# Performance work log

Hardware: AMD Instinct MI355X
Metric: run time of the kernel (lower is better)

The kernel has to match this reference:

```python
import jax, jax.numpy as jnp
import numpy as np

D = 128          # node_state_dim
N_NODES = 5000
WINDOW = 10
N_TOTAL = WINDOW * N_NODES
E = 131072       # structural (int) edges
T = 2            # message passing steps
HID = 1024


def setup_inputs() -> dict:
    key = jax.random.key(0)
    ks = jax.random.split(key, 20)
    ie = jax.random.randint(ks[0], (E, 3), 0, N_NODES, dtype=jnp.int32)
    int_edges = jnp.stack([ie[:, 0] % WINDOW, ie[:, 1], ie[:, 2]], axis=1)
    nodes = jax.random.randint(ks[1], (N_NODES,), 0, 10, dtype=jnp.int32)

    def init(k, shape, scale=0.05):
        return (jax.random.normal(k, shape, jnp.float32) * scale)

    params = dict(
        embed_table=init(ks[2], (10, D)),
        msg_W1=init(ks[3], (2 * D, HID)), msg_b1=jnp.zeros((HID,), jnp.float32),
        msg_W2=init(ks[4], (HID, D)), msg_b2=jnp.zeros((D,), jnp.float32),
        gru_int_W=init(ks[5], (D, 3 * D)), gru_int_U=init(ks[6], (D, 3 * D)),
        gru_int_b=jnp.zeros((2, 3 * D), jnp.float32),
        gru_temp_W=init(ks[7], (D, 3 * D)), gru_temp_U=init(ks[8], (D, 3 * D)),
        gru_temp_b=jnp.zeros((2, 3 * D), jnp.float32),
        ro_W1=init(ks[9], (D, HID)), ro_b1=jnp.zeros((HID,), jnp.float32),
        ro_W2=init(ks[10], (HID, 512)), ro_b2=jnp.zeros((512,), jnp.float32),
        ro_W3=init(ks[11], (512, 10)), ro_b3=jnp.zeros((10,), jnp.float32),
    )
    return {"int_edges": int_edges, "nodes": nodes, **params}


def _temp_edges():
    fwd_src = np.arange(0, N_TOTAL - N_NODES)
    fwd_dst = fwd_src + N_NODES
    bwd_src = np.arange(N_NODES, N_TOTAL)
    bwd_dst = bwd_src - N_NODES
    src = jnp.asarray(np.concatenate([fwd_src, bwd_src]), jnp.int32)
    dst = jnp.asarray(np.concatenate([fwd_dst, bwd_dst]), jnp.int32)
    return src, dst


def _gru(x, h, W, U, b):
    # Keras GRUCell, reset_after=True. x,h: [N,D]; W,U: [D,3D]; b: [2,3D]
    xg = x @ W + b[0]
    hg = h @ U + b[1]
    xz, xr, xh = jnp.split(xg, 3, axis=-1)
    hz, hr, hh = jnp.split(hg, 3, axis=-1)
    z = jax.nn.sigmoid(xz + hz)
    r = jax.nn.sigmoid(xr + hr)
    hcand = jnp.tanh(xh + r * hh)
    return z * h + (1.0 - z) * hcand


def _msg(x, W1, b1, W2, b2):
    # Dense(1024,relu) -> Dropout(inference: identity) -> Dense(D,relu)
    return jax.nn.relu(jax.nn.relu(x @ W1 + b1) @ W2 + b2)


def _seg_mean(x, idx, n):
    s = jax.ops.segment_sum(x, idx, num_segments=n)
    c = jax.ops.segment_sum(jnp.ones((x.shape[0],), x.dtype), idx, num_segments=n)
    return jnp.where(c[:, None] > 0, s / jnp.maximum(c, 1.0)[:, None], 0.0)


def reference(int_edges, nodes, embed_table, msg_W1, msg_b1, msg_W2, msg_b2,
              gru_int_W, gru_int_U, gru_int_b, gru_temp_W, gru_temp_U, gru_temp_b,
              ro_W1, ro_b1, ro_W2, ro_b2, ro_W3, ro_b3):
    node_idx = int_edges[:, 0] * N_NODES + int_edges[:, 1]        # [E]
    neigh_idx = int_edges[:, 0] * N_NODES + int_edges[:, 2]       # [E]
    t_src, t_dst = _temp_edges()

    h = embed_table[nodes]                                        # [n_nodes, D]
    h = jnp.repeat(h, WINDOW, axis=0)                             # [N_TOTAL, D]

    for _ in range(T):
        # structural edges
        m_in = jnp.concatenate([h[node_idx], h[neigh_idx]], axis=1)   # [E, 2D]
        m = _msg(m_in, msg_W1, msg_b1, msg_W2, msg_b2)                # [E, D]
        agg = _seg_mean(m, neigh_idx, N_TOTAL)                        # [N_TOTAL, D]
        h = _gru(agg, h, gru_int_W, gru_int_U, gru_int_b)
        # temporal edges
        tm_in = jnp.concatenate([h[t_src], h[t_dst]], axis=1)
        tm = _msg(tm_in, msg_W1, msg_b1, msg_W2, msg_b2)
        tagg = _seg_mean(tm, t_dst, N_TOTAL)
        h = _gru(tagg, h, gru_temp_W, gru_temp_U, gru_temp_b)

    # readout on first frame's nodes
    x = h[:N_NODES]
    x = jax.nn.relu(x @ ro_W1 + ro_b1)
    x = jax.nn.relu(x @ ro_W2 + ro_b2)
    return jax.nn.softmax(x @ ro_W3 + ro_b3, axis=-1)
```

## Files before the change

### kernel.cpp

```cpp
#include <hip/hip_runtime.h>
#include <math.h>

#define D 128
#define N_NODES 5000
#define WINDOW 10
#define N_TOTAL 50000
#define NE_INT 131072
#define NE_TMP 90000
#define NE_FWD (N_TOTAL - N_NODES)
#define HID 1024

typedef short bf16x8 __attribute__((ext_vector_type(8)));
typedef float f32x4 __attribute__((ext_vector_type(4)));

#define SA 264
#define SH 136
#define SK 136
#define SCAN_B 256

static __device__ __forceinline__ short f2bf(float f) {
    union { float f; unsigned u; } v; v.f = f;
    unsigned r = v.u + 0x7fffu + ((v.u >> 16) & 1u);
    return (short)(r >> 16);
}
static __device__ __forceinline__ float bf2f(short s) {
    union { unsigned u; float f; } v;
    v.u = ((unsigned)(unsigned short)s) << 16;
    return v.f;
}

__global__ void k_tcvt(const float* __restrict__ in, short* __restrict__ out, int K, int N) {
    int i = blockIdx.x * blockDim.x + threadIdx.x;
    if (i >= N * K) return;
    int n = i / K, k = i - n * K;
    out[i] = f2bf(in[(size_t)k * N + n]);
}

__global__ void k_init_h(const int* __restrict__ nodes, const float* __restrict__ embed,
                         float* __restrict__ h32, short* __restrict__ h16) {
    int i = blockIdx.x * blockDim.x + threadIdx.x;
    if (i >= N_TOTAL * D) return;
    int row = i >> 7;
    int c = i & 127;
    int n = nodes[row / WINDOW];
    float v = embed[n * D + c];
    h32[i] = v;
    h16[i] = f2bf(v);
}

__global__ void k_build_int_edges(const int* __restrict__ ie, int* __restrict__ src,
                                  int* __restrict__ dst, int* __restrict__ icnt) {
    int e = blockIdx.x * blockDim.x + threadIdx.x;
    if (e >= NE_INT) return;
    int t = ie[e * 3 + 0], a = ie[e * 3 + 1], b = ie[e * 3 + 2];
    int d = t * N_NODES + b;
    src[e] = t * N_NODES + a;
    dst[e] = d;
    atomicAdd(&icnt[d], 1);
}

__global__ void k_build_tmp_edges(int* __restrict__ src, int* __restrict__ dst) {
    int e = blockIdx.x * blockDim.x + threadIdx.x;
    if (e >= NE_TMP) return;
    int s, d;
    if (e < NE_FWD) { s = e; d = e + N_NODES; }
    else { int q = e - NE_FWD; s = q + N_NODES; d = q; }
    src[e] = s;
    dst[e] = d;
}

__global__ void k_scan_partial(const int* __restrict__ cnt, int* __restrict__ rowstart,
                               int* __restrict__ btot, int n) {
    __shared__ int s[SCAN_B];
    int tid = threadIdx.x;
    int i = blockIdx.x * SCAN_B + tid;
    int v = (i < n) ? cnt[i] : 0;
    s[tid] = v;
    __syncthreads();
    for (int off = 1; off < SCAN_B; off <<= 1) {
        int x = (tid >= off) ? s[tid - off] : 0;
        __syncthreads();
        s[tid] += x;
        __syncthreads();
    }
    if (i < n) rowstart[i] = s[tid] - v;
    if (tid == SCAN_B - 1) btot[blockIdx.x] = s[tid];
}

__global__ void k_scan_block(int* __restrict__ btot, int nb) {
    __shared__ int s[SCAN_B];
    int tid = threadIdx.x;
    int v = (tid < nb) ? btot[tid] : 0;
    s[tid] = v;
    __syncthreads();
    for (int off = 1; off < SCAN_B; off <<= 1) {
        int x = (tid >= off) ? s[tid - off] : 0;
        __syncthreads();
        s[tid] += x;
        __syncthreads();
    }
    if (tid < nb) btot[tid] = s[tid] - v;
}

__global__ void k_scan_add(int* __restrict__ rowstart, const int* __restrict__ btot,
                           int* __restrict__ cursor, int n, int total) {
    int i = blockIdx.x * blockDim.x + threadIdx.x;
    if (i < n) {
        int v = rowstart[i] + btot[i >> 8];
        rowstart[i] = v;
        cursor[i] = v;
    }
    if (i == 0) rowstart[n] = total;
}

__global__ void k_fill_csr(const int* __restrict__ dst, int nE, int* __restrict__ cursor,
                           int* __restrict__ eidx) {
    int e = blockIdx.x * blockDim.x + threadIdx.x;
    if (e >= nE) return;
    int p = atomicAdd(&cursor[dst[e]], 1);
    eidx[p] = e;
}

__global__ void __launch_bounds__(256, 2) k_msg_mfma(
    const short* __restrict__ h16, const int* __restrict__ src, const int* __restrict__ dst,
    int nE, const short* __restrict__ W1T, const float* __restrict__ b1,
    const short* __restrict__ W2T, const float* __restrict__ b2,
    short* __restrict__ m)
{
    __shared__ short Ain[64 * SA];
    __shared__ short Hid[64 * SH];

    int t = threadIdx.x;
    int e0 = blockIdx.x * 64;

    {
        int r = t >> 2, q = t & 3;
        int e = e0 + r;
        int ec = (e < nE) ? e : (nE - 1);
        int s = src[ec], d = dst[ec];
        const uint4* ps = (const uint4*)(h16 + (size_t)s * D);
        const uint4* pd = (const uint4*)(h16 + (size_t)d * D);
        uint4* ao = (uint4*)(Ain + r * SA);
#pragma unroll
        for (int i = 0; i < 8; ++i) {
            int g = i * 4 + q;
            ao[g] = (i < 4) ? ps[g] : pd[g - 16];
        }
    }
    __syncthreads();

    int w = t >> 6, lane = t & 63;
    int lm = lane & 15, lk = lane >> 4;

    f32x4 c2[2][4];
#pragma unroll
    for (int cs = 0; cs < 2; ++cs) {
        int out0 = w * 32 + cs * 16 + lk * 4;
#pragma unroll
        for (int et = 0; et < 4; ++et)
#pragma unroll
            for (int rg = 0; rg < 4; ++rg) c2[cs][et][rg] = b2[out0 + rg];
    }

    for (int hc = 0; hc < 8; ++hc) {
        f32x4 c1[2][4];
#pragma unroll
        for (int cs = 0; cs < 2; ++cs) {
            int ch0 = hc * 128 + (2 * w + cs) * 16 + lk * 4;
#pragma unroll
            for (int et = 0; et < 4; ++et)
#pragma unroll
                for (int rg = 0; rg < 4; ++rg) c1[cs][et][rg] = b1[ch0 + rg];
        }
#pragma unroll
        for (int kk = 0; kk < 8; ++kk) {
            int ko = kk * 32 + lk * 8;
            bf16x8 a0 = *(const bf16x8*)(W1T + (size_t)(hc * 128 + (2 * w) * 16 + lm) * 256 + ko);
            bf16x8 a1 = *(const bf16x8*)(W1T + (size_t)(hc * 128 + (2 * w + 1) * 16 + lm) * 256 + ko);
            bf16x8 bf[4];
#pragma unroll
            for (int et = 0; et < 4; ++et)
                bf[et] = *(const bf16x8*)(Ain + (et * 16 + lm) * SA + ko);
#pragma unroll
            for (int et = 0; et < 4; ++et) {
                c1[0][et] = __builtin_amdgcn_mfma_f32_16x16x32_bf16(a0, bf[et], c1[0][et], 0, 0, 0);
                c1[1][et] = __builtin_amdgcn_mfma_f32_16x16x32_bf16(a1, bf[et], c1[1][et], 0, 0, 0);
            }
        }
        __syncthreads();
#pragma unroll
        for (int cs = 0; cs < 2; ++cs) {
            int ch_in = (2 * w + cs) * 16 + lk * 4;
#pragma unroll
            for (int et = 0; et < 4; ++et) {
                int edge = et * 16 + lm;
                short4 sv;
                sv.x = f2bf(fmaxf(c1[cs][et][0], 0.f));
                sv.y = f2bf(fmaxf(c1[cs][et][1], 0.f));
                sv.z = f2bf(fmaxf(c1[cs][et][2], 0.f));
                sv.w = f2bf(fmaxf(c1[cs][et][3], 0.f));
                *(short4*)(Hid + edge * SH + ch_in) = sv;
            }
        }
        __syncthreads();
#pragma unroll
        for (int kk = 0; kk < 4; ++kk) {
            int ko = kk * 32 + lk * 8;
            bf16x8 a0 = *(const bf16x8*)(W2T + (size_t)(w * 32 + lm) * 1024 + hc * 128 + ko);
            bf16x8 a1 = *(const bf16x8*)(W2T + (size_t)(w * 32 + 16 + lm) * 1024 + hc * 128 + ko);
            bf16x8 bf[4];
#pragma unroll
            for (int et = 0; et < 4; ++et)
                bf[et] = *(const bf16x8*)(Hid + (et * 16 + lm) * SH + ko);
#pragma unroll
            for (int et = 0; et < 4; ++et) {
                c2[0][et] = __builtin_amdgcn_mfma_f32_16x16x32_bf16(a0, bf[et], c2[0][et], 0, 0, 0);
                c2[1][et] = __builtin_amdgcn_mfma_f32_16x16x32_bf16(a1, bf[et], c2[1][et], 0, 0, 0);
            }
        }
    }

#pragma unroll
    for (int et = 0; et < 4; ++et) {
        int edge = et * 16 + lm;
        int e = e0 + edge;
        if (e >= nE) continue;
        short* rowp = m + (size_t)e * 128;
#pragma unroll
        for (int cs = 0; cs < 2; ++cs) {
            int out0 = w * 32 + cs * 16 + lk * 4;
            short4 sv;
            sv.x = f2bf(fmaxf(c2[cs][et][0], 0.f));
            sv.y = f2bf(fmaxf(c2[cs][et][1], 0.f));
            sv.z = f2bf(fmaxf(c2[cs][et][2], 0.f));
            sv.w = f2bf(fmaxf(c2[cs][et][3], 0.f));
            *(short4*)(rowp + out0) = sv;
        }
    }
}

__global__ void __launch_bounds__(256, 2) k_gru_mfma(
    const short* __restrict__ m, const int* __restrict__ rowstart,
    const int* __restrict__ eidx, int mode,
    float* __restrict__ h32, short* __restrict__ h16,
    const short* __restrict__ WT, const short* __restrict__ UT,
    const float* __restrict__ b)
{
    __shared__ short Ax[64 * SK];
    __shared__ short Hx[64 * SK];
    int t = threadIdx.x;
    int r0 = blockIdx.x * 64;

    {
        int r = t >> 2, q = t & 3;
        int row = r0 + r;
        int rc = (row < N_TOTAL) ? row : (N_TOTAL - 1);
        const uint4* hp = (const uint4*)(h16 + (size_t)rc * D);
        uint4* hxo = (uint4*)(Hx + r * SK);
#pragma unroll
        for (int i = 0; i < 4; ++i) hxo[q * 4 + i] = hp[q * 4 + i];

        float acc[32];
#pragma unroll
        for (int i = 0; i < 32; ++i) acc[i] = 0.f;
        int deg = 0;
        if (row < N_TOTAL) {
            if (mode == 0) {
                int s0 = rowstart[row], s1 = rowstart[row + 1];
                deg = s1 - s0;
                for (int p = s0; p < s1; ++p) {
                    int e = eidx[p];
                    const uint4* mp = (const uint4*)(m + (size_t)e * 128 + q * 32);
#pragma unroll
                    for (int i = 0; i < 4; ++i) {
                        uint4 v = mp[i];
                        const short* sp = (const short*)&v;
#pragma unroll
                        for (int j = 0; j < 8; ++j) acc[i * 8 + j] += bf2f(sp[j]);
                    }
                }
            } else {
                if (row >= N_NODES) {
                    const uint4* mp = (const uint4*)(m + (size_t)(row - N_NODES) * 128 + q * 32);
                    ++deg;
#pragma unroll
                    for (int i = 0; i < 4; ++i) {
                        uint4 v = mp[i];
                        const short* sp = (const short*)&v;
#pragma unroll
                        for (int j = 0; j < 8; ++j) acc[i * 8 + j] += bf2f(sp[j]);
                    }
                }
                if (row < NE_FWD) {
                    const uint4* mp = (const uint4*)(m + (size_t)(NE_FWD + row) * 128 + q * 32);
                    ++deg;
#pragma unroll
                    for (int i = 0; i < 4; ++i) {
                        uint4 v = mp[i];
                        const short* sp = (const short*)&v;
#pragma unroll
                        for (int j = 0; j < 8; ++j) acc[i * 8 + j] += bf2f(sp[j]);
                    }
                }
            }
        }
        float inv = (deg > 0) ? 1.f / (float)deg : 0.f;
        uint4* axp = (uint4*)(Ax + r * SK + q * 32);
#pragma unroll
        for (int i = 0; i < 4; ++i) {
            union { uint4 u; short s[8]; } pk;
#pragma unroll
            for (int j = 0; j < 8; ++j) pk.s[j] = f2bf(acc[i * 8 + j] * inv);
            axp[i] = pk.u;
        }
    }
    __syncthreads();

    int w = t >> 6, lane = t & 63;
    int lm = lane & 15, lk = lane >> 4;

    for (int g = 0; g < 8; ++g) {
        int ch = g * 16 + lm;
        f32x4 cxz, cxr, cxh, chz, chr_, chh;
#pragma unroll
        for (int rg = 0; rg < 4; ++rg) {
            cxz[rg] = b[ch];        chz[rg] = b[384 + ch];
            cxr[rg] = b[128 + ch];  chr_[rg] = b[384 + 128 + ch];
            cxh[rg] = b[256 + ch];  chh[rg] = b[384 + 256 + ch];
        }
#pragma unroll
        for (int kk = 0; kk < 4; ++kk) {
            int ko = kk * 32 + lk * 8;
            bf16x8 ax = *(const bf16x8*)(Ax + (w * 16 + lm) * SK + ko);
            bf16x8 hx = *(const bf16x8*)(Hx + (w * 16 + lm) * SK + ko);
            bf16x8 bz = *(const bf16x8*)(WT + (size_t)(ch) * 128 + ko);
            bf16x8 br = *(const bf16x8*)(WT + (size_t)(128 + ch) * 128 + ko);
            bf16x8 bh = *(const bf16x8*)(WT + (size_t)(256 + ch) * 128 + ko);
            bf16x8 uz = *(const bf16x8*)(UT + (size_t)(ch) * 128 + ko);
            bf16x8 ur = *(const bf16x8*)(UT + (size_t)(128 + ch) * 128 + ko);
            bf16x8 uh = *(const bf16x8*)(UT + (size_t)(256 + ch) * 128 + ko);
            cxz = __builtin_amdgcn_mfma_f32_16x16x32_bf16(ax, bz, cxz, 0, 0, 0);
            cxr = __builtin_amdgcn_mfma_f32_16x16x32_bf16(ax, br, cxr, 0, 0, 0);
            cxh = __builtin_amdgcn_mfma_f32_16x16x32_bf16(ax, bh, cxh, 0, 0, 0);
            chz = __builtin_amdgcn_mfma_f32_16x16x32_bf16(hx, uz, chz, 0, 0, 0);
            chr_ = __builtin_amdgcn_mfma_f32_16x16x32_bf16(hx, ur, chr_, 0, 0, 0);
            chh = __builtin_amdgcn_mfma_f32_16x16x32_bf16(hx, uh, chh, 0, 0, 0);
        }
#pragma unroll
        for (int rg = 0; rg < 4; ++rg) {
            int row = r0 + w * 16 + lk * 4 + rg;
            if (row >= N_TOTAL) continue;
            float z = 1.f / (1.f + expf(-(cxz[rg] + chz[rg])));
            float r_ = 1.f / (1.f + expf(-(cxr[rg] + chr_[rg])));
            float hcv = tanhf(cxh[rg] + r_ * chh[rg]);
            size_t idx = (size_t)row * D + ch;
            float hold = h32[idx];
            float hnew = z * hold + (1.f - z) * hcv;
            h32[idx] = hnew;
            h16[idx] = f2bf(hnew);
        }
    }
}

__global__ void __launch_bounds__(256, 2) k_ro_mfma(
    const short* __restrict__ A16, const short* __restrict__ BT,
    const float* __restrict__ bias, float* __restrict__ C32, short* __restrict__ C16,
    int M, int N, int K)
{
    __shared__ short As[64 * SK];
    int t = threadIdx.x;
    int mb = blockIdx.y * 64;
    int nb = blockIdx.x * 128;
    int w = t >> 6, lane = t & 63;
    int lm = lane & 15, lk = lane >> 4;

    f32x4 acc[8];
#pragma unroll
    for (int nt = 0; nt < 8; ++nt) {
        float bv = bias[nb + nt * 16 + lm];
        acc[nt][0] = bv; acc[nt][1] = bv; acc[nt][2] = bv; acc[nt][3] = bv;
    }

    for (int kc = 0; kc < K; kc += 128) {
        __syncthreads();
        {
            int r = t >> 2, q = t & 3;
            int row = mb + r;
            int rc = (row < M) ? row : (M - 1);
            const uint4* ap = (const uint4*)(A16 + (size_t)rc * K + kc);
            uint4* ao = (uint4*)(As + r * SK);
#pragma unroll
            for (int i = 0; i < 4; ++i) ao[i * 4 + q] = ap[i * 4 + q];
        }
        __syncthreads();
#pragma unroll
        for (int kk = 0; kk < 4; ++kk) {
            int ko = kk * 32 + lk * 8;
            bf16x8 a = *(const bf16x8*)(As + (w * 16 + lm) * SK + ko);
#pragma unroll
            for (int nt = 0; nt < 8; ++nt) {
                bf16x8 bfr = *(const bf16x8*)(BT + (size_t)(nb + nt * 16 + lm) * K + kc + ko);
                acc[nt] = __builtin_amdgcn_mfma_f32_16x16x32_bf16(a, bfr, acc[nt], 0, 0, 0);
            }
        }
    }
#pragma unroll
    for (int nt = 0; nt < 8; ++nt) {
        int col = nb + nt * 16 + lm;
#pragma unroll
        for (int rg = 0; rg < 4; ++rg) {
            int row = mb + w * 16 + lk * 4 + rg;
            if (row >= M) continue;
            float v = fmaxf(acc[nt][rg], 0.f);
            if (C32) C32[(size_t)row * N + col] = v;
            if (C16) C16[(size_t)row * N + col] = f2bf(v);
        }
    }
}

__global__ void __launch_bounds__(64) k_logits_softmax(
    const float* __restrict__ r2, const float* __restrict__ W3,
    const float* __restrict__ b3, float* __restrict__ out)
{
    int row = blockIdx.x;
    int t = threadIdx.x;
    float p[10];
#pragma unroll
    for (int j = 0; j < 10; ++j) p[j] = 0.f;
    for (int k = t; k < 512; k += 64) {
        float v = r2[(size_t)row * 512 + k];
#pragma unroll
        for (int j = 0; j < 10; ++j) p[j] += v * W3[k * 10 + j];
    }
#pragma unroll
    for (int j = 0; j < 10; ++j) {
        float s = p[j];
        for (int off = 32; off > 0; off >>= 1) s += __shfl_down(s, off);
        p[j] = s;
    }
    if (t == 0) {
        float mx = -1e30f;
#pragma unroll
        for (int j = 0; j < 10; ++j) { p[j] += b3[j]; mx = fmaxf(mx, p[j]); }
        float sum = 0.f;
#pragma unroll
        for (int j = 0; j < 10; ++j) { p[j] = expf(p[j] - mx); sum += p[j]; }
        float inv = 1.f / sum;
#pragma unroll
        for (int j = 0; j < 10; ++j) out[(size_t)row * 10 + j] = p[j] * inv;
    }
}

extern "C" void kernel_launch(void* const* d_in, const int* in_sizes, int n_in,
                              void* d_out, int out_size, void* d_ws, size_t ws_size,
                              hipStream_t stream)
{
    const int*   ie    = (const int*)d_in[0];
    const int*   nodes = (const int*)d_in[1];
    const float* embed = (const float*)d_in[2];
    const float* mW1   = (const float*)d_in[3];
    const float* mb1   = (const float*)d_in[4];
    const float* mW2   = (const float*)d_in[5];
    const float* mb2   = (const float*)d_in[6];
    const float* giW   = (const float*)d_in[7];
    const float* giU   = (const float*)d_in[8];
    const float* gib   = (const float*)d_in[9];
    const float* gtW   = (const float*)d_in[10];
    const float* gtU   = (const float*)d_in[11];
    const float* gtb   = (const float*)d_in[12];
    const float* rW1   = (const float*)d_in[13];
    const float* rb1   = (const float*)d_in[14];
    const float* rW2   = (const float*)d_in[15];
    const float* rb2   = (const float*)d_in[16];
    const float* rW3   = (const float*)d_in[17];
    const float* rb3   = (const float*)d_in[18];
    float* out = (float*)d_out;

    char* ws = (char*)d_ws;
    size_t off = 0;
    auto alloc = [&](size_t bytes) {
        void* p = ws + off;
        off += (bytes + 255) & ~(size_t)255;
        return p;
    };
    float* h32   = (float*)alloc((size_t)N_TOTAL * D * 4);
    short* h16   = (short*)alloc((size_t)N_TOTAL * D * 2);
    short* m     = (short*)alloc((size_t)NE_INT * 128 * 2);
    int*   icnt  = (int*)alloc((size_t)N_TOTAL * 4);
    int*   rowst = (int*)alloc((size_t)(N_TOTAL + 1) * 4);
    int*   btot  = (int*)alloc(256 * 4);
    int*   curs  = (int*)alloc((size_t)N_TOTAL * 4);
    int*   eidx  = (int*)alloc((size_t)NE_INT * 4);
    int*   srcA  = (int*)alloc((size_t)NE_INT * 4);
    int*   dstA  = (int*)alloc((size_t)NE_INT * 4);
    int*   srcT  = (int*)alloc((size_t)NE_TMP * 4);
    int*   dstT  = (int*)alloc((size_t)NE_TMP * 4);
    short* mW1T  = (short*)alloc((size_t)HID * 256 * 2);
    short* mW2T  = (short*)alloc((size_t)D * HID * 2);
    short* giWT  = (short*)alloc((size_t)384 * D * 2);
    short* giUT  = (short*)alloc((size_t)384 * D * 2);
    short* gtWT  = (short*)alloc((size_t)384 * D * 2);
    short* gtUT  = (short*)alloc((size_t)384 * D * 2);
    short* rW1T  = (short*)alloc((size_t)HID * D * 2);
    short* rW2T  = (short*)alloc((size_t)512 * HID * 2);
    short* r1_16 = (short*)alloc((size_t)N_NODES * HID * 2);
    float* r2_32 = (float*)alloc((size_t)N_NODES * 512 * 4);

    auto tc = [&](const float* in, short* o, int K, int N) {
        k_tcvt<<<(N * K + 255) / 256, 256, 0, stream>>>(in, o, K, N);
    };
    tc(mW1, mW1T, 256, HID);
    tc(mW2, mW2T, HID, D);
    tc(giW, giWT, D, 384);
    tc(giU, giUT, D, 384);
    tc(gtW, gtWT, D, 384);
    tc(gtU, gtUT, D, 384);
    tc(rW1, rW1T, D, HID);
    tc(rW2, rW2T, HID, 512);

    hipMemsetAsync(icnt, 0, (size_t)N_TOTAL * 4, stream);
    k_init_h<<<(N_TOTAL * D + 255) / 256, 256, 0, stream>>>(nodes, embed, h32, h16);
    k_build_int_edges<<<(NE_INT + 255) / 256, 256, 0, stream>>>(ie, srcA, dstA, icnt);
    k_build_tmp_edges<<<(NE_TMP + 255) / 256, 256, 0, stream>>>(srcT, dstT);
    int nb = (N_TOTAL + SCAN_B - 1) / SCAN_B;
    k_scan_partial<<<nb, SCAN_B, 0, stream>>>(icnt, rowst, btot, N_TOTAL);
    k_scan_block<<<1, SCAN_B, 0, stream>>>(btot, nb);
    k_scan_add<<<nb, SCAN_B, 0, stream>>>(rowst, btot, curs, N_TOTAL, NE_INT);
    k_fill_csr<<<(NE_INT + 255) / 256, 256, 0, stream>>>(dstA, NE_INT, curs, eidx);

    int gmsgA = (NE_INT + 63) / 64;
    int gmsgT = (NE_TMP + 63) / 64;
    int ggru = (N_TOTAL + 63) / 64;
    for (int it = 0; it < 2; ++it) {
        k_msg_mfma<<<gmsgA, 256, 0, stream>>>(h16, srcA, dstA, NE_INT, mW1T, mb1, mW2T, mb2, m);
        k_gru_mfma<<<ggru, 256, 0, stream>>>(m, rowst, eidx, 0, h32, h16, giWT, giUT, gib);

        k_msg_mfma<<<gmsgT, 256, 0, stream>>>(h16, srcT, dstT, NE_TMP, mW1T, mb1, mW2T, mb2, m);
        k_gru_mfma<<<ggru, 256, 0, stream>>>(m, rowst, eidx, 1, h32, h16, gtWT, gtUT, gtb);
    }

    dim3 g1(HID / 128, (N_NODES + 63) / 64);
    k_ro_mfma<<<g1, 256, 0, stream>>>(h16, rW1T, rb1, (float*)nullptr, r1_16, N_NODES, HID, D);
    dim3 g2(512 / 128, (N_NODES + 63) / 64);
    k_ro_mfma<<<g2, 256, 0, stream>>>(r1_16, rW2T, rb2, r2_32, (short*)nullptr, N_NODES, 512, HID);
    k_logits_softmax<<<N_NODES, 64, 0, stream>>>(r2_32, rW3, rb3, out);
}
```

Baseline: 1.299 ms.

## Precompute per-node first-layer projections and gather them per edge

Splits the first message-MLP layer as [h_src,h_dst]@W1 = h_src@W1a + h_dst@W1b. Both halves are computed once per node into a 50000x2048 bf16 buffer, so each edge only gathers two 1024-wide rows, adds them and applies ReLU before the second GEMM. Structural edges are processed in CSR (dst-sorted) order, so the GRU aggregation reads messages contiguously without the eidx indirection. The change trades roughly 2.5x fewer first-layer FLOPs for a 200MB intermediate buffer that is written and then gathered from. It also adds an extra bf16 rounding before the sum, and falls back to the old path if the workspace is too small.

```diff
diff --git a/kernel.cpp b/kernel.cpp
--- a/kernel.cpp
+++ b/kernel.cpp
@@ -121,6 +121,178 @@
     eidx[p] = e;
 }
 
+__global__ void __launch_bounds__(256, 3) k_h12_mfma(
+    const short* __restrict__ h16, const short* __restrict__ W1cT,
+    const float* __restrict__ b1, short* __restrict__ H12)
+{
+    __shared__ short As[128 * SK];
+    int t = threadIdx.x;
+    int nb = blockIdx.x * 128;
+    int mb = blockIdx.y * 128;
+
+    {
+        int r = t >> 1, q = t & 1;
+        int row = mb + r;
+        int rc = (row < N_TOTAL) ? row : (N_TOTAL - 1);
+        const uint4* ap = (const uint4*)(h16 + (size_t)rc * D);
+        uint4* ao = (uint4*)(As + r * SK);
+#pragma unroll
+        for (int i = 0; i < 8; ++i) ao[q * 8 + i] = ap[q * 8 + i];
+    }
+    __syncthreads();
+
+    int w = t >> 6, lane = t & 63, lm = lane & 15, lk = lane >> 4;
+
+    f32x4 acc[2][8];
+#pragma unroll
+    for (int nt = 0; nt < 8; ++nt) {
+        int col = nb + nt * 16 + lm;
+        float bv = (col < HID) ? b1[col] : 0.f;
+#pragma unroll
+        for (int mt = 0; mt < 2; ++mt)
+#pragma unroll
+            for (int rg = 0; rg < 4; ++rg) acc[mt][nt][rg] = bv;
+    }
+#pragma unroll
+    for (int kk = 0; kk < 4; ++kk) {
+        int ko = kk * 32 + lk * 8;
+        bf16x8 a0 = *(const bf16x8*)(As + (w * 32 + lm) * SK + ko);
+        bf16x8 a1 = *(const bf16x8*)(As + (w * 32 + 16 + lm) * SK + ko);
+#pragma unroll
+        for (int nt = 0; nt < 8; ++nt) {
+            bf16x8 bfr = *(const bf16x8*)(W1cT + (size_t)(nb + nt * 16 + lm) * D + ko);
+            acc[0][nt] = __builtin_amdgcn_mfma_f32_16x16x32_bf16(a0, bfr, acc[0][nt], 0, 0, 0);
+            acc[1][nt] = __builtin_amdgcn_mfma_f32_16x16x32_bf16(a1, bfr, acc[1][nt], 0, 0, 0);
+        }
+    }
+#pragma unroll
+    for (int mt = 0; mt < 2; ++mt)
+#pragma unroll
+        for (int rg = 0; rg < 4; ++rg) {
+            int row = mb + w * 32 + mt * 16 + lk * 4 + rg;
+            if (row >= N_TOTAL) continue;
+            short* op = H12 + (size_t)row * 2048 + nb;
+#pragma unroll
+            for (int nt = 0; nt < 8; ++nt)
+                op[nt * 16 + lm] = f2bf(acc[mt][nt][rg]);
+        }
+}
+
+__global__ void __launch_bounds__(256, 3) k_msg2_mfma(
+    const short* __restrict__ H12, const int* __restrict__ perm,
+    const int* __restrict__ src, const int* __restrict__ dst, int nE,
+    const short* __restrict__ W2T, const float* __restrict__ b2,
+    short* __restrict__ m)
+{
+    __shared__ short S[2][64 * SH];
+    __shared__ int es[64], ed[64];
+    int t = threadIdx.x;
+    int p0 = blockIdx.x * 64;
+
+    if (t < 64) {
+        int p = p0 + t;
+        int pc = (p < nE) ? p : (nE - 1);
+        int e = perm ? perm[pc] : pc;
+        es[t] = src[e];
+        ed[t] = dst[e];
+    }
+    __syncthreads();
+
+    int w = t >> 6, lane = t & 63, lm = lane & 15, lk = lane >> 4;
+    int r = t >> 2, q = t & 3;
+    const short* p1 = H12 + (size_t)es[r] * 2048 + q * 32;
+    const short* p2 = H12 + (size_t)ed[r] * 2048 + 1024 + q * 32;
+
+    uint4 ra[4], rb[4];
+#pragma unroll
+    for (int i = 0; i < 4; ++i) {
+        ra[i] = *(const uint4*)(p1 + i * 8);
+        rb[i] = *(const uint4*)(p2 + i * 8);
+    }
+
+    f32x4 c2[2][4];
+#pragma unroll
+    for (int cs = 0; cs < 2; ++cs) {
+        int out0 = w * 32 + cs * 16 + lk * 4;
+#pragma unroll
+        for (int et = 0; et < 4; ++et)
+#pragma unroll
+            for (int rg = 0; rg < 4; ++rg) c2[cs][et][rg] = b2[out0 + rg];
+    }
+
+    {
+        uint4* sp = (uint4*)(S[0] + r * SH + q * 32);
+#pragma unroll
+        for (int i = 0; i < 4; ++i) {
+            union { uint4 u; short s[8]; } pa, pb, po;
+            pa.u = ra[i]; pb.u = rb[i];
+#pragma unroll
+            for (int j = 0; j < 8; ++j)
+                po.s[j] = f2bf(fmaxf(bf2f(pa.s[j]) + bf2f(pb.s[j]), 0.f));
+            sp[i] = po.u;
+        }
+    }
+
+    for (int hc = 0; hc < 8; ++hc) {
+        int cur = hc & 1;
+        __syncthreads();
+        if (hc < 7) {
+            const short* q1 = p1 + (hc + 1) * 128;
+            const short* q2 = p2 + (hc + 1) * 128;
+#pragma unroll
+            for (int i = 0; i < 4; ++i) {
+                ra[i] = *(const uint4*)(q1 + i * 8);
+                rb[i] = *(const uint4*)(q2 + i * 8);
+            }
+        }
+#pragma unroll
+        for (int kk = 0; kk < 4; ++kk) {
+            int ko = kk * 32 + lk * 8;
+            bf16x8 a0 = *(const bf16x8*)(W2T + (size_t)(w * 32 + lm) * 1024 + hc * 128 + ko);
+            bf16x8 a1 = *(const bf16x8*)(W2T + (size_t)(w * 32 + 16 + lm) * 1024 + hc * 128 + ko);
+            bf16x8 bf[4];
+#pragma unroll
+            for (int et = 0; et < 4; ++et)
+                bf[et] = *(const bf16x8*)(S[cur] + (et * 16 + lm) * SH + ko);
+#pragma unroll
+            for (int et = 0; et < 4; ++et) {
+                c2[0][et] = __builtin_amdgcn_mfma_f32_16x16x32_bf16(a0, bf[et], c2[0][et], 0, 0, 0);
+                c2[1][et] = __builtin_amdgcn_mfma_f32_16x16x32_bf16(a1, bf[et], c2[1][et], 0, 0, 0);
+            }
+        }
+        if (hc < 7) {
+            uint4* sp = (uint4*)(S[cur ^ 1] + r * SH + q * 32);
+#pragma unroll
+            for (int i = 0; i < 4; ++i) {
+                union { uint4 u; short s[8]; } pa, pb, po;
+                pa.u = ra[i]; pb.u = rb[i];
+#pragma unroll
+                for (int j = 0; j < 8; ++j)
+                    po.s[j] = f2bf(fmaxf(bf2f(pa.s[j]) + bf2f(pb.s[j]), 0.f));
+                sp[i] = po.u;
+            }
+        }
+    }
+
+#pragma unroll
+    for (int et = 0; et < 4; ++et) {
+        int edge = et * 16 + lm;
+        int p = p0 + edge;
+        if (p >= nE) continue;
+        short* rowp = m + (size_t)p * 128;
+#pragma unroll
+        for (int cs = 0; cs < 2; ++cs) {
+            int out0 = w * 32 + cs * 16 + lk * 4;
+            short4 sv;
+            sv.x = f2bf(fmaxf(c2[cs][et][0], 0.f));
+            sv.y = f2bf(fmaxf(c2[cs][et][1], 0.f));
+            sv.z = f2bf(fmaxf(c2[cs][et][2], 0.f));
+            sv.w = f2bf(fmaxf(c2[cs][et][3], 0.f));
+            *(short4*)(rowp + out0) = sv;
+        }
+    }
+}
+
 __global__ void __launch_bounds__(256, 2) k_msg_mfma(
     const short* __restrict__ h16, const int* __restrict__ src, const int* __restrict__ dst,
     int nE, const short* __restrict__ W1T, const float* __restrict__ b1,
@@ -241,7 +413,7 @@
 
 __global__ void __launch_bounds__(256, 2) k_gru_mfma(
     const short* __restrict__ m, const int* __restrict__ rowstart,
-    const int* __restrict__ eidx, int mode,
+    const int* __restrict__ midx, int mode,
     float* __restrict__ h32, short* __restrict__ h16,
     const short* __restrict__ WT, const short* __restrict__ UT,
     const float* __restrict__ b)
@@ -269,7 +441,7 @@
                 int s0 = rowstart[row], s1 = rowstart[row + 1];
                 deg = s1 - s0;
                 for (int p = s0; p < s1; ++p) {
-                    int e = eidx[p];
+                    int e = midx ? midx[p] : p;
                     const uint4* mp = (const uint4*)(m + (size_t)e * 128 + q * 32);
 #pragma unroll
                     for (int i = 0; i < 4; ++i) {
@@ -505,6 +677,11 @@
     short* rW2T  = (short*)alloc((size_t)512 * HID * 2);
     short* r1_16 = (short*)alloc((size_t)N_NODES * HID * 2);
     float* r2_32 = (float*)alloc((size_t)N_NODES * 512 * 4);
+    short* W1cT  = (short*)alloc((size_t)2048 * D * 2);
+
+    size_t h12_bytes = (size_t)N_TOTAL * 2048 * 2;
+    bool useH12 = (off + h12_bytes <= ws_size);
+    short* H12 = useH12 ? (short*)alloc(h12_bytes) : nullptr;
 
     auto tc = [&](const float* in, short* o, int K, int N) {
         k_tcvt<<<(N * K + 255) / 256, 256, 0, stream>>>(in, o, K, N);
@@ -517,6 +694,10 @@
     tc(gtU, gtUT, D, 384);
     tc(rW1, rW1T, D, HID);
     tc(rW2, rW2T, HID, 512);
+    if (useH12) {
+        tc(mW1, W1cT, D, HID);
+        tc(mW1 + (size_t)D * HID, W1cT + (size_t)HID * D, D, HID);
+    }
 
     hipMemsetAsync(icnt, 0, (size_t)N_TOTAL * 4, stream);
     k_init_h<<<(N_TOTAL * D + 255) / 256, 256, 0, stream>>>(nodes, embed, h32, h16);
@@ -531,12 +712,23 @@
     int gmsgA = (NE_INT + 63) / 64;
     int gmsgT = (NE_TMP + 63) / 64;
     int ggru = (N_TOTAL + 63) / 64;
+    dim3 gh12(2048 / 128, (N_TOTAL + 127) / 128);
     for (int it = 0; it < 2; ++it) {
-        k_msg_mfma<<<gmsgA, 256, 0, stream>>>(h16, srcA, dstA, NE_INT, mW1T, mb1, mW2T, mb2, m);
-        k_gru_mfma<<<ggru, 256, 0, stream>>>(m, rowst, eidx, 0, h32, h16, giWT, giUT, gib);
-
-        k_msg_mfma<<<gmsgT, 256, 0, stream>>>(h16, srcT, dstT, NE_TMP, mW1T, mb1, mW2T, mb2, m);
-        k_gru_mfma<<<ggru, 256, 0, stream>>>(m, rowst, eidx, 1, h32, h16, gtWT, gtUT, gtb);
+        if (useH12) {
+            k_h12_mfma<<<gh12, 256, 0, stream>>>(h16, W1cT, mb1, H12);
+            k_msg2_mfma<<<gmsgA, 256, 0, stream>>>(H12, eidx, srcA, dstA, NE_INT, mW2T, mb2, m);
+            k_gru_mfma<<<ggru, 256, 0, stream>>>(m, rowst, (const int*)nullptr, 0, h32, h16, giWT, giUT, gib);
+
+            k_h12_mfma<<<gh12, 256, 0, stream>>>(h16, W1cT, mb1, H12);
+            k_msg2_mfma<<<gmsgT, 256, 0, stream>>>(H12, (const int*)nullptr, srcT, dstT, NE_TMP, mW2T, mb2, m);
+            k_gru_mfma<<<ggru, 256, 0, stream>>>(m, rowst, (const int*)nullptr, 1, h32, h16, gtWT, gtUT, gtb);
+        } else {
+            k_msg_mfma<<<gmsgA, 256, 0, stream>>>(h16, srcA, dstA, NE_INT, mW1T, mb1, mW2T, mb2, m);
+            k_gru_mfma<<<ggru, 256, 0, stream>>>(m, rowst, eidx, 0, h32, h16, giWT, giUT, gib);
+
+            k_msg_mfma<<<gmsgT, 256, 0, stream>>>(h16, srcT, dstT, NE_TMP, mW1T, mb1, mW2T, mb2, m);
+            k_gru_mfma<<<ggru, 256, 0, stream>>>(m, rowst, eidx, 1, h32, h16, gtWT, gtUT, gtb);
+        }
     }
 
     dim3 g1(HID / 128, (N_NODES + 63) / 64);
```

Result: no change. 1.297 ms (-0.2%).

## Software-pipeline message MLP layers and scatter messages into CSR order

Applied to the files above, without the earlier changes.

The message kernel now computes the first-layer MFMA block for hidden chunk hc+1 interleaved with the second-layer MFMAs for chunk hc. This is meant to hide the dependency stall between the two GEMM stages. Message rows are also written straight into CSR slot order through a precomputed position map, so the GRU aggregation reads contiguous rows instead of going through eidx. The bf16 unpacking in aggregation now uses 32-bit shifts and masks. The costs are higher register pressure from keeping two accumulator sets live, and scattered stores in the message kernel.

```diff
diff --git a/kernel.cpp b/kernel.cpp
--- a/kernel.cpp
+++ b/kernel.cpp
@@ -27,6 +27,12 @@
     union { unsigned u; float f; } v;
     v.u = ((unsigned)(unsigned short)s) << 16;
     return v.f;
+}
+static __device__ __forceinline__ float lo_bf(unsigned u) {
+    union { unsigned u; float f; } v; v.u = u << 16; return v.f;
+}
+static __device__ __forceinline__ float hi_bf(unsigned u) {
+    union { unsigned u; float f; } v; v.u = u & 0xffff0000u; return v.f;
 }
 
 __global__ void k_tcvt(const float* __restrict__ in, short* __restrict__ out, int K, int N) {
@@ -114,16 +120,17 @@
 }
 
 __global__ void k_fill_csr(const int* __restrict__ dst, int nE, int* __restrict__ cursor,
-                           int* __restrict__ eidx) {
+                           int* __restrict__ pmap) {
     int e = blockIdx.x * blockDim.x + threadIdx.x;
     if (e >= nE) return;
     int p = atomicAdd(&cursor[dst[e]], 1);
-    eidx[p] = e;
+    pmap[e] = p;
 }
 
 __global__ void __launch_bounds__(256, 2) k_msg_mfma(
     const short* __restrict__ h16, const int* __restrict__ src, const int* __restrict__ dst,
-    int nE, const short* __restrict__ W1T, const float* __restrict__ b1,
+    const int* __restrict__ pmap, int nE,
+    const short* __restrict__ W1T, const float* __restrict__ b1,
     const short* __restrict__ W2T, const float* __restrict__ b2,
     short* __restrict__ m)
 {
@@ -162,31 +169,32 @@
             for (int rg = 0; rg < 4; ++rg) c2[cs][et][rg] = b2[out0 + rg];
     }
 
+    f32x4 c1[2][4];
+#pragma unroll
+    for (int cs = 0; cs < 2; ++cs) {
+        int ch0 = (2 * w + cs) * 16 + lk * 4;
+#pragma unroll
+        for (int et = 0; et < 4; ++et)
+#pragma unroll
+            for (int rg = 0; rg < 4; ++rg) c1[cs][et][rg] = b1[ch0 + rg];
+    }
+#pragma unroll
+    for (int kk = 0; kk < 8; ++kk) {
+        int ko = kk * 32 + lk * 8;
+        bf16x8 a0 = *(const bf16x8*)(W1T + (size_t)((2 * w) * 16 + lm) * 256 + ko);
+        bf16x8 a1 = *(const bf16x8*)(W1T + (size_t)((2 * w + 1) * 16 + lm) * 256 + ko);
+        bf16x8 bf[4];
+#pragma unroll
+        for (int et = 0; et < 4; ++et)
+            bf[et] = *(const bf16x8*)(Ain + (et * 16 + lm) * SA + ko);
+#pragma unroll
+        for (int et = 0; et < 4; ++et) {
+            c1[0][et] = __builtin_amdgcn_mfma_f32_16x16x32_bf16(a0, bf[et], c1[0][et], 0, 0, 0);
+            c1[1][et] = __builtin_amdgcn_mfma_f32_16x16x32_bf16(a1, bf[et], c1[1][et], 0, 0, 0);
+        }
+    }
+
     for (int hc = 0; hc < 8; ++hc) {
-        f32x4 c1[2][4];
-#pragma unroll
-        for (int cs = 0; cs < 2; ++cs) {
-            int ch0 = hc * 128 + (2 * w + cs) * 16 + lk * 4;
-#pragma unroll
-            for (int et = 0; et < 4; ++et)
-#pragma unroll
-                for (int rg = 0; rg < 4; ++rg) c1[cs][et][rg] = b1[ch0 + rg];
-        }
-#pragma unroll
-        for (int kk = 0; kk < 8; ++kk) {
-            int ko = kk * 32 + lk * 8;
-            bf16x8 a0 = *(const bf16x8*)(W1T + (size_t)(hc * 128 + (2 * w) * 16 + lm) * 256 + ko);
-            bf16x8 a1 = *(const bf16x8*)(W1T + (size_t)(hc * 128 + (2 * w + 1) * 16 + lm) * 256 + ko);
-            bf16x8 bf[4];
-#pragma unroll
-            for (int et = 0; et < 4; ++et)
-                bf[et] = *(const bf16x8*)(Ain + (et * 16 + lm) * SA + ko);
-#pragma unroll
-            for (int et = 0; et < 4; ++et) {
-                c1[0][et] = __builtin_amdgcn_mfma_f32_16x16x32_bf16(a0, bf[et], c1[0][et], 0, 0, 0);
-                c1[1][et] = __builtin_amdgcn_mfma_f32_16x16x32_bf16(a1, bf[et], c1[1][et], 0, 0, 0);
-            }
-        }
         __syncthreads();
 #pragma unroll
         for (int cs = 0; cs < 2; ++cs) {
@@ -203,19 +211,45 @@
             }
         }
         __syncthreads();
-#pragma unroll
-        for (int kk = 0; kk < 4; ++kk) {
+
+        if (hc < 7) {
+#pragma unroll
+            for (int cs = 0; cs < 2; ++cs) {
+                int ch0 = (hc + 1) * 128 + (2 * w + cs) * 16 + lk * 4;
+#pragma unroll
+                for (int et = 0; et < 4; ++et)
+#pragma unroll
+                    for (int rg = 0; rg < 4; ++rg) c1[cs][et][rg] = b1[ch0 + rg];
+            }
+        }
+#pragma unroll
+        for (int kk = 0; kk < 8; ++kk) {
             int ko = kk * 32 + lk * 8;
-            bf16x8 a0 = *(const bf16x8*)(W2T + (size_t)(w * 32 + lm) * 1024 + hc * 128 + ko);
-            bf16x8 a1 = *(const bf16x8*)(W2T + (size_t)(w * 32 + 16 + lm) * 1024 + hc * 128 + ko);
-            bf16x8 bf[4];
-#pragma unroll
-            for (int et = 0; et < 4; ++et)
-                bf[et] = *(const bf16x8*)(Hid + (et * 16 + lm) * SH + ko);
-#pragma unroll
-            for (int et = 0; et < 4; ++et) {
-                c2[0][et] = __builtin_amdgcn_mfma_f32_16x16x32_bf16(a0, bf[et], c2[0][et], 0, 0, 0);
-                c2[1][et] = __builtin_amdgcn_mfma_f32_16x16x32_bf16(a1, bf[et], c2[1][et], 0, 0, 0);
+            if (kk < 4) {
+                bf16x8 a0 = *(const bf16x8*)(W2T + (size_t)(w * 32 + lm) * 1024 + hc * 128 + ko);
+                bf16x8 a1 = *(const bf16x8*)(W2T + (size_t)(w * 32 + 16 + lm) * 1024 + hc * 128 + ko);
+                bf16x8 bf[4];
+#pragma unroll
+                for (int et = 0; et < 4; ++et)
+                    bf[et] = *(const bf16x8*)(Hid + (et * 16 + lm) * SH + ko);
+#pragma unroll
+                for (int et = 0; et < 4; ++et) {
+                    c2[0][et] = __builtin_amdgcn_mfma_f32_16x16x32_bf16(a0, bf[et], c2[0][et], 0, 0, 0);
+                    c2[1][et] = __builtin_amdgcn_mfma_f32_16x16x32_bf16(a1, bf[et], c2[1][et], 0, 0, 0);
+                }
+            }
+            if (hc < 7) {
+                bf16x8 a0 = *(const bf16x8*)(W1T + (size_t)((hc + 1) * 128 + (2 * w) * 16 + lm) * 256 + ko);
+                bf16x8 a1 = *(const bf16x8*)(W1T + (size_t)((hc + 1) * 128 + (2 * w + 1) * 16 + lm) * 256 + ko);
+                bf16x8 bf[4];
+#pragma unroll
+                for (int et = 0; et < 4; ++et)
+                    bf[et] = *(const bf16x8*)(Ain + (et * 16 + lm) * SA + ko);
+#pragma unroll
+                for (int et = 0; et < 4; ++et) {
+                    c1[0][et] = __builtin_amdgcn_mfma_f32_16x16x32_bf16(a0, bf[et], c1[0][et], 0, 0, 0);
+                    c1[1][et] = __builtin_amdgcn_mfma_f32_16x16x32_bf16(a1, bf[et], c1[1][et], 0, 0, 0);
+                }
             }
         }
     }
@@ -225,7 +259,8 @@
         int edge = et * 16 + lm;
         int e = e0 + edge;
         if (e >= nE) continue;
-        short* rowp = m + (size_t)e * 128;
+        int slot = pmap ? pmap[e] : e;
+        short* rowp = m + (size_t)slot * 128;
 #pragma unroll
         for (int cs = 0; cs < 2; ++cs) {
             int out0 = w * 32 + cs * 16 + lk * 4;
@@ -240,8 +275,7 @@
 }
 
 __global__ void __launch_bounds__(256, 2) k_gru_mfma(
-    const short* __restrict__ m, const int* __restrict__ rowstart,
-    const int* __restrict__ eidx, int mode,
+    const short* __restrict__ m, const int* __restrict__ rowstart, int mode,
     float* __restrict__ h32, short* __restrict__ h16,
     const short* __restrict__ WT, const short* __restrict__ UT,
     const float* __restrict__ b)
@@ -269,14 +303,16 @@
                 int s0 = rowstart[row], s1 = rowstart[row + 1];
                 deg = s1 - s0;
                 for (int p = s0; p < s1; ++p) {
-                    int e = eidx[p];
-                    const uint4* mp = (const uint4*)(m + (size_t)e * 128 + q * 32);
+                    const uint4* mp = (const uint4*)(m + (size_t)p * 128 + q * 32);
 #pragma unroll
                     for (int i = 0; i < 4; ++i) {
                         uint4 v = mp[i];
-                        const short* sp = (const short*)&v;
-#pragma unroll
-                        for (int j = 0; j < 8; ++j) acc[i * 8 + j] += bf2f(sp[j]);
+                        unsigned ua[4] = {v.x, v.y, v.z, v.w};
+#pragma unroll
+                        for (int j = 0; j < 4; ++j) {
+                            acc[i * 8 + 2 * j]     += lo_bf(ua[j]);
+                            acc[i * 8 + 2 * j + 1] += hi_bf(ua[j]);
+                        }
                     }
                 }
             } else {
@@ -286,9 +322,12 @@
 #pragma unroll
                     for (int i = 0; i < 4; ++i) {
                         uint4 v = mp[i];
-                        const short* sp = (const short*)&v;
-#pragma unroll
-                        for (int j = 0; j < 8; ++j) acc[i * 8 + j] += bf2f(sp[j]);
+                        unsigned ua[4] = {v.x, v.y, v.z, v.w};
+#pragma unroll
+                        for (int j = 0; j < 4; ++j) {
+                            acc[i * 8 + 2 * j]     += lo_bf(ua[j]);
+                            acc[i * 8 + 2 * j + 1] += hi_bf(ua[j]);
+                        }
                     }
                 }
                 if (row < NE_FWD) {
@@ -297,9 +336,12 @@
 #pragma unroll
                     for (int i = 0; i < 4; ++i) {
                         uint4 v = mp[i];
-                        const short* sp = (const short*)&v;
-#pragma unroll
-                        for (int j = 0; j < 8; ++j) acc[i * 8 + j] += bf2f(sp[j]);
+                        unsigned ua[4] = {v.x, v.y, v.z, v.w};
+#pragma unroll
+                        for (int j = 0; j < 4; ++j) {
+                            acc[i * 8 + 2 * j]     += lo_bf(ua[j]);
+                            acc[i * 8 + 2 * j + 1] += hi_bf(ua[j]);
+                        }
                     }
                 }
             }
@@ -490,7 +532,7 @@
     int*   rowst = (int*)alloc((size_t)(N_TOTAL + 1) * 4);
     int*   btot  = (int*)alloc(256 * 4);
     int*   curs  = (int*)alloc((size_t)N_TOTAL * 4);
-    int*   eidx  = (int*)alloc((size_t)NE_INT * 4);
+    int*   pmap  = (int*)alloc((size_t)NE_INT * 4);
     int*   srcA  = (int*)alloc((size_t)NE_INT * 4);
     int*   dstA  = (int*)alloc((size_t)NE_INT * 4);
     int*   srcT  = (int*)alloc((size_t)NE_TMP * 4);
@@ -526,17 +568,17 @@
     k_scan_partial<<<nb, SCAN_B, 0, stream>>>(icnt, rowst, btot, N_TOTAL);
     k_scan_block<<<1, SCAN_B, 0, stream>>>(btot, nb);
     k_scan_add<<<nb, SCAN_B, 0, stream>>>(rowst, btot, curs, N_TOTAL, NE_INT);
-    k_fill_csr<<<(NE_INT + 255) / 256, 256, 0, stream>>>(dstA, NE_INT, curs, eidx);
+    k_fill_csr<<<(NE_INT + 255) / 256, 256, 0, stream>>>(dstA, NE_INT, curs, pmap);
 
     int gmsgA = (NE_INT + 63) / 64;
     int gmsgT = (NE_TMP + 63) / 64;
     int ggru = (N_TOTAL + 63) / 64;
     for (int it = 0; it < 2; ++it) {
-        k_msg_mfma<<<gmsgA, 256, 0, stream>>>(h16, srcA, dstA, NE_INT, mW1T, mb1, mW2T, mb2, m);
-        k_gru_mfma<<<ggru, 256, 0, stream>>>(m, rowst, eidx, 0, h32, h16, giWT, giUT, gib);
-
-        k_msg_mfma<<<gmsgT, 256, 0, stream>>>(h16, srcT, dstT, NE_TMP, mW1T, mb1, mW2T, mb2, m);
-        k_gru_mfma<<<ggru, 256, 0, stream>>>(m, rowst, eidx, 1, h32, h16, gtWT, gtUT, gtb);
+        k_msg_mfma<<<gmsgA, 256, 0, stream>>>(h16, srcA, dstA, pmap, NE_INT, mW1T, mb1, mW2T, mb2, m);
+        k_gru_mfma<<<ggru, 256, 0, stream>>>(m, rowst, 0, h32, h16, giWT, giUT, gib);
+
+        k_msg_mfma<<<gmsgT, 256, 0, stream>>>(h16, srcT, dstT, (const int*)nullptr, NE_TMP, mW1T, mb1, mW2T, mb2, m);
+        k_gru_mfma<<<ggru, 256, 0, stream>>>(m, rowst, 1, h32, h16, gtWT, gtUT, gtb);
     }
 
     dim3 g1(HID / 128, (N_NODES + 63) / 64);
```

Measured after the change: 1.298 ms. About the same (-0.1%).
